# Optimization experiments

Measured on AMD Instinct MI355X. Metric: run time of the kernel, lower is better.

Reference implementation:

```python
import jax, jax.numpy as jnp
import numpy as np

B, S, D, DS = 8, 2048, 1024, 128
TEMP = 1.0
C = 8.0


def setup_inputs() -> dict:
    key = jax.random.key(0)
    ks = jax.random.split(key, 8)
    s_in = 1.0 / np.sqrt(D)
    s_st = 1.0 / np.sqrt(DS)
    return {
        "x": jax.random.normal(ks[0], (B, S, D), jnp.float32),
        "W_k": jax.random.normal(ks[1], (DS, D), jnp.float32) * s_in,
        "W_v": jax.random.normal(ks[2], (DS, D), jnp.float32) * s_in,
        "W_q": jax.random.normal(ks[3], (DS, D), jnp.float32) * s_in,
        "W_alpha_w": jax.random.normal(ks[4], (DS, D), jnp.float32) * s_in,
        "W_alpha_b": jnp.zeros((DS,), jnp.float32),
        "lambda_param": jax.random.uniform(ks[5], (DS,), jnp.float32, 4.0, 9.0),
        "W_o": jax.random.normal(ks[6], (D, DS), jnp.float32) * s_st,
        "norm_weight": jnp.ones((DS,), jnp.float32),
    }


def _l2norm(z):
    # matches F.normalize(..., dim=-1) with eps=1e-12
    n = jnp.linalg.norm(z, axis=-1, keepdims=True)
    return z / jnp.maximum(n, 1e-12)


def reference(x, W_k, W_v, W_q, W_alpha_w, W_alpha_b, lambda_param, W_o, norm_weight):
    # projections
    k = _l2norm(x @ W_k.T)                      # [B,S,DS]
    v = x @ W_v.T                               # [B,S,DS]
    q = _l2norm(x @ W_q.T)                      # [B,S,DS]
    r = jax.nn.sigmoid(x @ W_alpha_w.T + W_alpha_b)
    log_a = jnp.log(jax.nn.sigmoid(lambda_param) + 1e-8)  # [DS]
    alpha = jnp.exp(C * r * log_a)              # [B,S,DS], data-dependent decay

    H0 = jnp.zeros((B, DS, DS), x.dtype)        # state indexed [b, k, v]

    def step(H, inp):
        k_t, v_t, q_t, a_t = inp                # each [B,DS]
        # surprise: prediction error against current state
        pred = jnp.einsum('bk,bkv->bv', q_t, H)
        err = jnp.sum((v_t - pred) ** 2, axis=-1, keepdims=True)  # [B,1]
        sur = jax.nn.sigmoid(err / (TEMP + 1e-6))                 # [B,1]
        # delta rule: k (x) v - k (x) (k^T H) = k (x) (v - k^T H)
        k_proj = jnp.einsum('bk,bkv->bv', k_t, H)
        delta = k_t[:, :, None] * (v_t - k_proj)[:, None, :]      # [B,DS,DS]
        a_e = a_t[:, :, None]                                     # decay on k-axis
        H = a_e * H + (1.0 - a_e) * (sur[:, :, None] * delta)
        y = jnp.einsum('bk,bkv->bv', q_t, H)
        return H, y

    seq = (k.transpose(1, 0, 2), v.transpose(1, 0, 2),
           q.transpose(1, 0, 2), alpha.transpose(1, 0, 2))
    _, ys = jax.lax.scan(step, H0, seq)         # ys: [S,B,DS]
    y = ys.transpose(1, 0, 2)                   # [B,S,DS]

    # RMSNorm (computed in fp32, like the torch module)
    yf = y.astype(jnp.float32)
    yn = yf * jax.lax.rsqrt(jnp.mean(yf * yf, axis=-1, keepdims=True) + 1e-6)
    yn = (yn * norm_weight).astype(y.dtype)
    return yn @ W_o.T                           # [B,S,D]
```

## Files before the change

kernel.cpp:

```cpp
#include <hip/hip_runtime.h>
#include <math.h>

#define S_LEN 2048
#define B_SZ 8
#define D_IN 1024
#define DS_ 128
#define INV_TEMP (1.0f/1.000001f)
#define LBUF 712

#define BAR_LDS() asm volatile("s_waitcnt lgkmcnt(0)\n\ts_barrier" ::: "memory")

#define DPPADD(x, ctrl) { int t_ = __builtin_amdgcn_update_dpp( \
    0, __float_as_int(x), ctrl, 0xF, 0xF, false); x += __int_as_float(t_); }
#define ROWSUM(x) { DPPADD(x, 0x128) DPPADD(x, 0x124) DPPADD(x, 0x122) DPPADD(x, 0x121) }
#define ROWSUM4(v4) { ROWSUM(v4.x) ROWSUM(v4.y) ROWSUM(v4.z) ROWSUM(v4.w) }

__global__ __launch_bounds__(256) void proj_gemm(
    const float* __restrict__ X,
    const float* __restrict__ Wk, const float* __restrict__ Wv,
    const float* __restrict__ Wq, const float* __restrict__ Wa,
    float* __restrict__ P)
{
    __shared__ __align__(16) float As[32][68];
    __shared__ __align__(16) float Bs[32][68];
    const int tid = threadIdx.x;
    const int m0 = blockIdx.x * 64;
    const int n0 = blockIdx.y * 64;
    const int lr = tid >> 3;
    const int lk4 = tid & 7;

    const float* wrows[2];
#pragma unroll
    for (int i = 0; i < 2; i++) {
        int nn = n0 + lr + i * 32;
        const float* w;
        if      (nn < 128) w = Wk + (size_t)nn * D_IN;
        else if (nn < 256) w = Wv + (size_t)(nn - 128) * D_IN;
        else if (nn < 384) w = Wq + (size_t)(nn - 256) * D_IN;
        else               w = Wa + (size_t)(nn - 384) * D_IN;
        wrows[i] = w;
    }
    const int ty = tid >> 4, tx = tid & 15;
    float acc[4][4];
#pragma unroll
    for (int i = 0; i < 4; i++)
#pragma unroll
        for (int j = 0; j < 4; j++) acc[i][j] = 0.f;

    for (int k0 = 0; k0 < D_IN; k0 += 32) {
#pragma unroll
        for (int i = 0; i < 2; i++) {
            int m = lr + i * 32;
            float4 a4 = *(const float4*)(X + (size_t)(m0 + m) * D_IN + k0 + lk4 * 4);
            As[lk4*4+0][m] = a4.x; As[lk4*4+1][m] = a4.y;
            As[lk4*4+2][m] = a4.z; As[lk4*4+3][m] = a4.w;
            float4 b4 = *(const float4*)(wrows[i] + k0 + lk4 * 4);
            Bs[lk4*4+0][m] = b4.x; Bs[lk4*4+1][m] = b4.y;
            Bs[lk4*4+2][m] = b4.z; Bs[lk4*4+3][m] = b4.w;
        }
        __syncthreads();
#pragma unroll
        for (int kk = 0; kk < 32; kk++) {
            float4 a4 = *(const float4*)(&As[kk][ty * 4]);
            float4 b4 = *(const float4*)(&Bs[kk][tx * 4]);
            float a[4] = {a4.x, a4.y, a4.z, a4.w};
            float b[4] = {b4.x, b4.y, b4.z, b4.w};
#pragma unroll
            for (int i = 0; i < 4; i++)
#pragma unroll
                for (int j = 0; j < 4; j++)
                    acc[i][j] = fmaf(a[i], b[j], acc[i][j]);
        }
        __syncthreads();
    }
#pragma unroll
    for (int i = 0; i < 4; i++) {
        float4 o; o.x = acc[i][0]; o.y = acc[i][1]; o.z = acc[i][2]; o.w = acc[i][3];
        *(float4*)(P + (size_t)(m0 + ty * 4 + i) * 512 + n0 + tx * 4) = o;
    }
}

__global__ __launch_bounds__(128) void postproc(
    float* __restrict__ P, float* __restrict__ G,
    const float* __restrict__ bA, const float* __restrict__ lam)
{
    const int tok = blockIdx.x, i = threadIdx.x;
    float* row = P + (size_t)tok * 512;
    float kr = row[i], qr = row[256 + i], rr = row[384 + i];
    float ks = kr * kr, qs = qr * qr;
#pragma unroll
    for (int m = 1; m < 64; m <<= 1) { ks += __shfl_xor(ks, m); qs += __shfl_xor(qs, m); }
    __shared__ float sb[6];
    if ((i & 63) == 0) { sb[(i >> 6) * 2] = ks; sb[(i >> 6) * 2 + 1] = qs; }
    __syncthreads();
    float kinv = 1.0f / fmaxf(sqrtf(sb[0] + sb[2]), 1e-12f);
    float qinv = 1.0f / fmaxf(sqrtf(sb[1] + sb[3]), 1e-12f);
    float kn = kr * kinv, qn = qr * qinv;
    float sr = 1.0f / (1.0f + __expf(-(rr + bA[i])));
    float sl = 1.0f / (1.0f + __expf(-lam[i]));
    float la = logf(sl + 1e-8f);
    float al = __expf(8.0f * sr * la);
    row[i] = kn; row[256 + i] = qn; row[384 + i] = al;
    float gi = qn * (1.0f - al) * kn;
#pragma unroll
    for (int m = 1; m < 64; m <<= 1) gi += __shfl_xor(gi, m);
    if ((i & 63) == 0) sb[4 + (i >> 6)] = gi;
    __syncthreads();
    if (i == 0) G[tok] = sb[4] + sb[5];
}

__global__ __launch_bounds__(512, 2) void recurrence(
    const float* __restrict__ P, const float* __restrict__ G, float* __restrict__ Y)
{
    const int b = blockIdx.x;
    const int tid = threadIdx.x;
    const int c = tid & 15;
    const int vp = tid >> 4;
    const int lane = tid & 63;
    const int wave = tid >> 6;
    const int co = c * 12;

    __shared__ __align__(16) float Pbuf[3][LBUF];
    __shared__ __align__(16) float errw[2][8];

    const float* Pb = P + (size_t)b * S_LEN * 512;
    const float* Gb = G + (size_t)b * S_LEN;
    float* Yb = Y + (size_t)b * S_LEN * DS_;

    float4 H0={0,0,0,0},H1={0,0,0,0},H2={0,0,0,0},H3={0,0,0,0},
           H4={0,0,0,0},H5={0,0,0,0},H6={0,0,0,0},H7={0,0,0,0};

    const bool isP = tid < 256;
    const bool isG = (tid == 256);
    int spos = 0;
    if (isP) {
        int i = tid * 2, s = i >> 7, idx = i & 127, cp = (idx >> 3) * 12 + (idx & 7);
        spos = (s == 0) ? cp : (s == 1) ? (576 + idx) : (s == 2) ? (192 + cp) : (384 + cp);
    }

    float2 rp0 = {0.f, 0.f}, rp1 = {0.f, 0.f};
    float rg0 = 0.f, rg1 = 0.f;
    if (isP) { rp0 = *(const float2*)(Pb + tid * 2); rp1 = *(const float2*)(Pb + 512 + tid * 2); }
    if (isG) { rg0 = Gb[0]; rg1 = Gb[1]; }
    if (isP) *(float2*)(&Pbuf[0][spos]) = rp0;
    if (isG) Pbuf[0][704] = rg0;
    __syncthreads();

#define DOTJ(qs, ks, zs, Hj) { \
    pr.x = fmaf(qs, Hj.x, pr.x); pr.y = fmaf(qs, Hj.y, pr.y); \
    pr.z = fmaf(qs, Hj.z, pr.z); pr.w = fmaf(qs, Hj.w, pr.w); \
    kp.x = fmaf(ks, Hj.x, kp.x); kp.y = fmaf(ks, Hj.y, kp.y); \
    kp.z = fmaf(ks, Hj.z, kp.z); kp.w = fmaf(ks, Hj.w, kp.w); \
    ya.x = fmaf(zs, Hj.x, ya.x); ya.y = fmaf(zs, Hj.y, ya.y); \
    ya.z = fmaf(zs, Hj.z, ya.z); ya.w = fmaf(zs, Hj.w, ya.w); }

#define UPDJ(as_, ws_, Hj) { \
    Hj.x = fmaf(as_, Hj.x, ws_ * sd.x); Hj.y = fmaf(as_, Hj.y, ws_ * sd.y); \
    Hj.z = fmaf(as_, Hj.z, ws_ * sd.z); Hj.w = fmaf(as_, Hj.w, ws_ * sd.w); }

#define STEP(T, PAR, RPS, RGS, RPL, RGL) { \
    float* cb = &Pbuf[(T) % 3][0]; \
    const float4 k0 = *(const float4*)(cb + co); \
    const float4 k1 = *(const float4*)(cb + co + 4); \
    const float4 q0 = *(const float4*)(cb + 192 + co); \
    const float4 q1 = *(const float4*)(cb + 192 + co + 4); \
    const float4 a0 = *(const float4*)(cb + 384 + co); \
    const float4 a1 = *(const float4*)(cb + 384 + co + 4); \
    const float4 vt = *(const float4*)(cb + 576 + vp * 4); \
    const float g = cb[704]; \
    float4 z0, z1, w0, w1; \
    z0.x = q0.x * a0.x; z0.y = q0.y * a0.y; z0.z = q0.z * a0.z; z0.w = q0.w * a0.w; \
    z1.x = q1.x * a1.x; z1.y = q1.y * a1.y; z1.z = q1.z * a1.z; z1.w = q1.w * a1.w; \
    w0.x = fmaf(-k0.x, a0.x, k0.x); w0.y = fmaf(-k0.y, a0.y, k0.y); \
    w0.z = fmaf(-k0.z, a0.z, k0.z); w0.w = fmaf(-k0.w, a0.w, k0.w); \
    w1.x = fmaf(-k1.x, a1.x, k1.x); w1.y = fmaf(-k1.y, a1.y, k1.y); \
    w1.z = fmaf(-k1.z, a1.z, k1.z); w1.w = fmaf(-k1.w, a1.w, k1.w); \
    float4 pr = {0,0,0,0}, kp = {0,0,0,0}, ya = {0,0,0,0}; \
    DOTJ(q0.x, k0.x, z0.x, H0) DOTJ(q0.y, k0.y, z0.y, H1) \
    DOTJ(q0.z, k0.z, z0.z, H2) DOTJ(q0.w, k0.w, z0.w, H3) \
    DOTJ(q1.x, k1.x, z1.x, H4) DOTJ(q1.y, k1.y, z1.y, H5) \
    DOTJ(q1.z, k1.z, z1.z, H6) DOTJ(q1.w, k1.w, z1.w, H7) \
    ROWSUM4(pr) ROWSUM4(kp) ROWSUM4(ya) \
    float4 d4; d4.x = vt.x - kp.x; d4.y = vt.y - kp.y; \
    d4.z = vt.z - kp.z; d4.w = vt.w - kp.w; \
    float ex = vt.x - pr.x, ey = vt.y - pr.y, ez = vt.z - pr.z, ew = vt.w - pr.w; \
    float ep = fmaf(ex, ex, fmaf(ey, ey, fmaf(ez, ez, ew * ew))); \
    ep += __shfl_xor(ep, 16); ep += __shfl_xor(ep, 32); \
    if (lane == 0) errw[PAR][wave] = ep; \
    if ((T) + 1 < S_LEN) { \
        if (isP) *(float2*)(&Pbuf[((T) + 1) % 3][spos]) = RPS; \
        if (isG) Pbuf[((T) + 1) % 3][704] = RGS; } \
    if ((T) + 2 < S_LEN) { \
        if (isP) RPL = *(const float2*)(Pb + (size_t)((T) + 2) * 512 + tid * 2); \
        if (isG) RGL = Gb[(T) + 2]; } \
    BAR_LDS(); \
    const float4 ea = *(const float4*)(&errw[PAR][0]); \
    const float4 eb = *(const float4*)(&errw[PAR][4]); \
    float err = ((ea.x + ea.y) + (ea.z + ea.w)) + ((eb.x + eb.y) + (eb.z + eb.w)); \
    float sur = 1.0f / (1.0f + __expf(-err * INV_TEMP)); \
    float4 sd; sd.x = sur * d4.x; sd.y = sur * d4.y; \
    sd.z = sur * d4.z; sd.w = sur * d4.w; \
    if (c == 0) { \
        float sg = sur * g; float4 y4; \
        y4.x = fmaf(sg, d4.x, ya.x); y4.y = fmaf(sg, d4.y, ya.y); \
        y4.z = fmaf(sg, d4.z, ya.z); y4.w = fmaf(sg, d4.w, ya.w); \
        *(float4*)(Yb + (size_t)(T) * DS_ + vp * 4) = y4; } \
    UPDJ(a0.x, w0.x, H0) UPDJ(a0.y, w0.y, H1) \
    UPDJ(a0.z, w0.z, H2) UPDJ(a0.w, w0.w, H3) \
    UPDJ(a1.x, w1.x, H4) UPDJ(a1.y, w1.y, H5) \
    UPDJ(a1.z, w1.z, H6) UPDJ(a1.w, w1.w, H7) \
}

    for (int t = 0; t < S_LEN; t += 2) {
        STEP(t,     0, rp1, rg1, rp0, rg0)
        STEP(t + 1, 1, rp0, rg0, rp1, rg1)
    }
#undef DOTJ
#undef UPDJ
#undef STEP
}

__global__ __launch_bounds__(128) void rmsnorm(
    float* __restrict__ Y, const float* __restrict__ nw)
{
    const int tok = blockIdx.x, i = threadIdx.x;
    float y = Y[(size_t)tok * DS_ + i];
    float s = y * y;
#pragma unroll
    for (int m = 1; m < 64; m <<= 1) s += __shfl_xor(s, m);
    __shared__ float sb[2];
    if ((i & 63) == 0) sb[i >> 6] = s;
    __syncthreads();
    float ms = (sb[0] + sb[1]) * (1.0f / 128.0f);
    Y[(size_t)tok * DS_ + i] = y * rsqrtf(ms + 1e-6f) * nw[i];
}

__global__ __launch_bounds__(256) void out_gemm(
    const float* __restrict__ Yn, const float* __restrict__ Wo, float* __restrict__ Out)
{
    __shared__ __align__(16) float As[32][68];
    __shared__ __align__(16) float Bs[32][68];
    const int tid = threadIdx.x;
    const int m0 = blockIdx.x * 64;
    const int n0 = blockIdx.y * 64;
    const int lr = tid >> 3;
    const int lk4 = tid & 7;
    const int ty = tid >> 4, tx = tid & 15;
    float acc[4][4];
#pragma unroll
    for (int i = 0; i < 4; i++)
#pragma unroll
        for (int j = 0; j < 4; j++) acc[i][j] = 0.f;

    for (int k0 = 0; k0 < DS_; k0 += 32) {
#pragma unroll
        for (int i = 0; i < 2; i++) {
            int m = lr + i * 32;
            float4 a4 = *(const float4*)(Yn + (size_t)(m0 + m) * DS_ + k0 + lk4 * 4);
            As[lk4*4+0][m] = a4.x; As[lk4*4+1][m] = a4.y;
            As[lk4*4+2][m] = a4.z; As[lk4*4+3][m] = a4.w;
            float4 b4 = *(const float4*)(Wo + (size_t)(n0 + m) * DS_ + k0 + lk4 * 4);
            Bs[lk4*4+0][m] = b4.x; Bs[lk4*4+1][m] = b4.y;
            Bs[lk4*4+2][m] = b4.z; Bs[lk4*4+3][m] = b4.w;
        }
        __syncthreads();
#pragma unroll
        for (int kk = 0; kk < 32; kk++) {
            float4 a4 = *(const float4*)(&As[kk][ty * 4]);
            float4 b4 = *(const float4*)(&Bs[kk][tx * 4]);
            float a[4] = {a4.x, a4.y, a4.z, a4.w};
            float b[4] = {b4.x, b4.y, b4.z, b4.w};
#pragma unroll
            for (int i = 0; i < 4; i++)
#pragma unroll
                for (int j = 0; j < 4; j++)
                    acc[i][j] = fmaf(a[i], b[j], acc[i][j]);
        }
        __syncthreads();
    }
#pragma unroll
    for (int i = 0; i < 4; i++) {
        float4 o; o.x = acc[i][0]; o.y = acc[i][1]; o.z = acc[i][2]; o.w = acc[i][3];
        *(float4*)(Out + (size_t)(m0 + ty * 4 + i) * 1024 + n0 + tx * 4) = o;
    }
}

extern "C" void kernel_launch(void* const* d_in, const int* in_sizes, int n_in,
                              void* d_out, int out_size, void* d_ws, size_t ws_size,
                              hipStream_t stream)
{
    const float* x   = (const float*)d_in[0];
    const float* Wk  = (const float*)d_in[1];
    const float* Wv  = (const float*)d_in[2];
    const float* Wq  = (const float*)d_in[3];
    const float* Waw = (const float*)d_in[4];
    const float* Wab = (const float*)d_in[5];
    const float* lam = (const float*)d_in[6];
    const float* Wo  = (const float*)d_in[7];
    const float* nw  = (const float*)d_in[8];
    float* out = (float*)d_out;

    const size_t NTOK = (size_t)B_SZ * S_LEN;
    float* P  = (float*)d_ws;
    float* G  = P + NTOK * 512;
    float* Y  = G + NTOK;

    proj_gemm<<<dim3(NTOK / 64, 512 / 64), 256, 0, stream>>>(x, Wk, Wv, Wq, Waw, P);
    postproc<<<NTOK, 128, 0, stream>>>(P, G, Wab, lam);
    recurrence<<<B_SZ, 512, 0, stream>>>(P, G, Y);
    rmsnorm<<<NTOK, 128, 0, stream>>>(Y, nw);
    out_gemm<<<dim3(NTOK / 64, 1024 / 64), 256, 0, stream>>>(Y, Wo, out);
}
```

Measured before the change: 2.744 ms.

## Split recurrence across two blocks per batch with cross-block error exchange

```diff
diff --git a/kernel.cpp b/kernel.cpp
--- a/kernel.cpp
+++ b/kernel.cpp
@@ -7,13 +7,13 @@
 #define DS_ 128
 #define INV_TEMP (1.0f/1.000001f)
 #define LBUF 712
+#define NBLK 16
 
 #define BAR_LDS() asm volatile("s_waitcnt lgkmcnt(0)\n\ts_barrier" ::: "memory")
 
 #define DPPADD(x, ctrl) { int t_ = __builtin_amdgcn_update_dpp( \
     0, __float_as_int(x), ctrl, 0xF, 0xF, false); x += __int_as_float(t_); }
 #define ROWSUM(x) { DPPADD(x, 0x128) DPPADD(x, 0x124) DPPADD(x, 0x122) DPPADD(x, 0x121) }
-#define ROWSUM4(v4) { ROWSUM(v4.x) ROWSUM(v4.y) ROWSUM(v4.z) ROWSUM(v4.w) }
 
 __global__ __launch_bounds__(256) void proj_gemm(
     const float* __restrict__ X,
@@ -110,25 +110,32 @@
 }
 
 __global__ __launch_bounds__(512, 2) void recurrence(
-    const float* __restrict__ P, const float* __restrict__ G, float* __restrict__ Y)
-{
-    const int b = blockIdx.x;
+    const float* __restrict__ P, const float* __restrict__ G,
+    float* __restrict__ Y, float* __restrict__ EB)
+{
+    const int bx = blockIdx.x;
+    const int b = bx & 7;
+    const int half = bx >> 3;
     const int tid = threadIdx.x;
     const int c = tid & 15;
     const int vp = tid >> 4;
     const int lane = tid & 63;
     const int wave = tid >> 6;
     const int co = c * 12;
+    const int voff = 576 + half * 64 + vp * 2;
 
     __shared__ __align__(16) float Pbuf[3][LBUF];
     __shared__ __align__(16) float errw[2][8];
 
     const float* Pb = P + (size_t)b * S_LEN * 512;
     const float* Gb = G + (size_t)b * S_LEN;
-    float* Yb = Y + (size_t)b * S_LEN * DS_;
-
-    float4 H0={0,0,0,0},H1={0,0,0,0},H2={0,0,0,0},H3={0,0,0,0},
-           H4={0,0,0,0},H5={0,0,0,0},H6={0,0,0,0},H7={0,0,0,0};
+    float* Yb = Y + (size_t)b * S_LEN * DS_ + half * 64;
+    float* own = EB + (size_t)bx * S_LEN;
+    const float* peer = EB + (size_t)(bx ^ 8) * S_LEN;
+
+    float2 H[8];
+#pragma unroll
+    for (int j = 0; j < 8; j++) { H[j].x = 0.f; H[j].y = 0.f; }
 
     const bool isP = tid < 256;
     const bool isG = (tid == 256);
@@ -146,47 +153,34 @@
     if (isG) Pbuf[0][704] = rg0;
     __syncthreads();
 
-#define DOTJ(qs, ks, zs, Hj) { \
-    pr.x = fmaf(qs, Hj.x, pr.x); pr.y = fmaf(qs, Hj.y, pr.y); \
-    pr.z = fmaf(qs, Hj.z, pr.z); pr.w = fmaf(qs, Hj.w, pr.w); \
-    kp.x = fmaf(ks, Hj.x, kp.x); kp.y = fmaf(ks, Hj.y, kp.y); \
-    kp.z = fmaf(ks, Hj.z, kp.z); kp.w = fmaf(ks, Hj.w, kp.w); \
-    ya.x = fmaf(zs, Hj.x, ya.x); ya.y = fmaf(zs, Hj.y, ya.y); \
-    ya.z = fmaf(zs, Hj.z, ya.z); ya.w = fmaf(zs, Hj.w, ya.w); }
-
-#define UPDJ(as_, ws_, Hj) { \
-    Hj.x = fmaf(as_, Hj.x, ws_ * sd.x); Hj.y = fmaf(as_, Hj.y, ws_ * sd.y); \
-    Hj.z = fmaf(as_, Hj.z, ws_ * sd.z); Hj.w = fmaf(as_, Hj.w, ws_ * sd.w); }
+    float4 k0, k1, q0, q1, a0, a1; float2 vt; float g;
+#define LOADREGS(T) { float* cb = &Pbuf[(T) % 3][0]; \
+    k0 = *(const float4*)(cb + co);       k1 = *(const float4*)(cb + co + 4); \
+    q0 = *(const float4*)(cb + 192 + co); q1 = *(const float4*)(cb + 192 + co + 4); \
+    a0 = *(const float4*)(cb + 384 + co); a1 = *(const float4*)(cb + 384 + co + 4); \
+    vt = *(const float2*)(cb + voff);     g  = cb[704]; }
+
+    LOADREGS(0)
 
 #define STEP(T, PAR, RPS, RGS, RPL, RGL) { \
-    float* cb = &Pbuf[(T) % 3][0]; \
-    const float4 k0 = *(const float4*)(cb + co); \
-    const float4 k1 = *(const float4*)(cb + co + 4); \
-    const float4 q0 = *(const float4*)(cb + 192 + co); \
-    const float4 q1 = *(const float4*)(cb + 192 + co + 4); \
-    const float4 a0 = *(const float4*)(cb + 384 + co); \
-    const float4 a1 = *(const float4*)(cb + 384 + co + 4); \
-    const float4 vt = *(const float4*)(cb + 576 + vp * 4); \
-    const float g = cb[704]; \
-    float4 z0, z1, w0, w1; \
-    z0.x = q0.x * a0.x; z0.y = q0.y * a0.y; z0.z = q0.z * a0.z; z0.w = q0.w * a0.w; \
-    z1.x = q1.x * a1.x; z1.y = q1.y * a1.y; z1.z = q1.z * a1.z; z1.w = q1.w * a1.w; \
-    w0.x = fmaf(-k0.x, a0.x, k0.x); w0.y = fmaf(-k0.y, a0.y, k0.y); \
-    w0.z = fmaf(-k0.z, a0.z, k0.z); w0.w = fmaf(-k0.w, a0.w, k0.w); \
-    w1.x = fmaf(-k1.x, a1.x, k1.x); w1.y = fmaf(-k1.y, a1.y, k1.y); \
-    w1.z = fmaf(-k1.z, a1.z, k1.z); w1.w = fmaf(-k1.w, a1.w, k1.w); \
-    float4 pr = {0,0,0,0}, kp = {0,0,0,0}, ya = {0,0,0,0}; \
-    DOTJ(q0.x, k0.x, z0.x, H0) DOTJ(q0.y, k0.y, z0.y, H1) \
-    DOTJ(q0.z, k0.z, z0.z, H2) DOTJ(q0.w, k0.w, z0.w, H3) \
-    DOTJ(q1.x, k1.x, z1.x, H4) DOTJ(q1.y, k1.y, z1.y, H5) \
-    DOTJ(q1.z, k1.z, z1.z, H6) DOTJ(q1.w, k1.w, z1.w, H7) \
-    ROWSUM4(pr) ROWSUM4(kp) ROWSUM4(ya) \
-    float4 d4; d4.x = vt.x - kp.x; d4.y = vt.y - kp.y; \
-    d4.z = vt.z - kp.z; d4.w = vt.w - kp.w; \
-    float ex = vt.x - pr.x, ey = vt.y - pr.y, ez = vt.z - pr.z, ew = vt.w - pr.w; \
-    float ep = fmaf(ex, ex, fmaf(ey, ey, fmaf(ez, ez, ew * ew))); \
+    float kk[8] = {k0.x,k0.y,k0.z,k0.w,k1.x,k1.y,k1.z,k1.w}; \
+    float qq[8] = {q0.x,q0.y,q0.z,q0.w,q1.x,q1.y,q1.z,q1.w}; \
+    float aa[8] = {a0.x,a0.y,a0.z,a0.w,a1.x,a1.y,a1.z,a1.w}; \
+    float zz[8], ww[8]; \
+    _Pragma("unroll") for (int j = 0; j < 8; j++) { \
+        zz[j] = qq[j] * aa[j]; ww[j] = fmaf(-kk[j], aa[j], kk[j]); } \
+    float2 pr = {0.f,0.f}, kp = {0.f,0.f}, ya = {0.f,0.f}; \
+    _Pragma("unroll") for (int j = 0; j < 8; j++) { \
+        pr.x = fmaf(qq[j], H[j].x, pr.x); pr.y = fmaf(qq[j], H[j].y, pr.y); \
+        kp.x = fmaf(kk[j], H[j].x, kp.x); kp.y = fmaf(kk[j], H[j].y, kp.y); \
+        ya.x = fmaf(zz[j], H[j].x, ya.x); ya.y = fmaf(zz[j], H[j].y, ya.y); } \
+    ROWSUM(pr.x) ROWSUM(pr.y) ROWSUM(kp.x) ROWSUM(kp.y) ROWSUM(ya.x) ROWSUM(ya.y) \
+    float ex = vt.x - pr.x, ey = vt.y - pr.y; \
+    float ep = fmaf(ex, ex, ey * ey); \
     ep += __shfl_xor(ep, 16); ep += __shfl_xor(ep, 32); \
     if (lane == 0) errw[PAR][wave] = ep; \
+    float2 d2; d2.x = vt.x - kp.x; d2.y = vt.y - kp.y; \
+    const float gcur = g; const float2 yac = ya; \
     if ((T) + 1 < S_LEN) { \
         if (isP) *(float2*)(&Pbuf[((T) + 1) % 3][spos]) = RPS; \
         if (isG) Pbuf[((T) + 1) % 3][704] = RGS; } \
@@ -194,30 +188,33 @@
         if (isP) RPL = *(const float2*)(Pb + (size_t)((T) + 2) * 512 + tid * 2); \
         if (isG) RGL = Gb[(T) + 2]; } \
     BAR_LDS(); \
-    const float4 ea = *(const float4*)(&errw[PAR][0]); \
-    const float4 eb = *(const float4*)(&errw[PAR][4]); \
-    float err = ((ea.x + ea.y) + (ea.z + ea.w)) + ((eb.x + eb.y) + (eb.z + eb.w)); \
+    const float4 ea  = *(const float4*)(&errw[PAR][0]); \
+    const float4 eb2 = *(const float4*)(&errw[PAR][4]); \
+    float el = ((ea.x + ea.y) + (ea.z + ea.w)) + ((eb2.x + eb2.y) + (eb2.z + eb2.w)); \
+    if (tid == 0) __hip_atomic_store(own + (T), el + 1.0f, \
+        __ATOMIC_RELAXED, __HIP_MEMORY_SCOPE_AGENT); \
+    _Pragma("unroll") for (int j = 0; j < 8; j++) { H[j].x *= aa[j]; H[j].y *= aa[j]; } \
+    if ((T) + 1 < S_LEN) LOADREGS((T) + 1) \
+    float pv; \
+    do { pv = __hip_atomic_load(peer + (T), \
+        __ATOMIC_RELAXED, __HIP_MEMORY_SCOPE_AGENT); } while (pv == 0.0f); \
+    float err = el + (pv - 1.0f); \
     float sur = 1.0f / (1.0f + __expf(-err * INV_TEMP)); \
-    float4 sd; sd.x = sur * d4.x; sd.y = sur * d4.y; \
-    sd.z = sur * d4.z; sd.w = sur * d4.w; \
+    float2 sd; sd.x = sur * d2.x; sd.y = sur * d2.y; \
+    _Pragma("unroll") for (int j = 0; j < 8; j++) { \
+        H[j].x = fmaf(ww[j], sd.x, H[j].x); H[j].y = fmaf(ww[j], sd.y, H[j].y); } \
     if (c == 0) { \
-        float sg = sur * g; float4 y4; \
-        y4.x = fmaf(sg, d4.x, ya.x); y4.y = fmaf(sg, d4.y, ya.y); \
-        y4.z = fmaf(sg, d4.z, ya.z); y4.w = fmaf(sg, d4.w, ya.w); \
-        *(float4*)(Yb + (size_t)(T) * DS_ + vp * 4) = y4; } \
-    UPDJ(a0.x, w0.x, H0) UPDJ(a0.y, w0.y, H1) \
-    UPDJ(a0.z, w0.z, H2) UPDJ(a0.w, w0.w, H3) \
-    UPDJ(a1.x, w1.x, H4) UPDJ(a1.y, w1.y, H5) \
-    UPDJ(a1.z, w1.z, H6) UPDJ(a1.w, w1.w, H7) \
+        float sg = sur * gcur; float2 y2; \
+        y2.x = fmaf(sg, d2.x, yac.x); y2.y = fmaf(sg, d2.y, yac.y); \
+        *(float2*)(Yb + (size_t)(T) * DS_ + vp * 2) = y2; } \
 }
 
     for (int t = 0; t < S_LEN; t += 2) {
         STEP(t,     0, rp1, rg1, rp0, rg0)
         STEP(t + 1, 1, rp0, rg0, rp1, rg1)
     }
-#undef DOTJ
-#undef UPDJ
 #undef STEP
+#undef LOADREGS
 }
 
 __global__ __launch_bounds__(128) void rmsnorm(
@@ -304,10 +301,12 @@
     float* P  = (float*)d_ws;
     float* G  = P + NTOK * 512;
     float* Y  = G + NTOK;
-
+    float* EB = Y + NTOK * 128;
+
+    hipMemsetAsync(EB, 0, (size_t)NBLK * S_LEN * sizeof(float), stream);
     proj_gemm<<<dim3(NTOK / 64, 512 / 64), 256, 0, stream>>>(x, Wk, Wv, Wq, Waw, P);
     postproc<<<NTOK, 128, 0, stream>>>(P, G, Wab, lam);
-    recurrence<<<B_SZ, 512, 0, stream>>>(P, G, Y);
+    recurrence<<<NBLK, 512, 0, stream>>>(P, G, Y, EB);
     rmsnorm<<<NTOK, 128, 0, stream>>>(Y, nw);
     out_gemm<<<dim3(NTOK / 64, 1024 / 64), 256, 0, stream>>>(Y, Wo, out);
 }
```

Result: slower. 2.985 ms (+8.8%).

## Enlarge GEMM tiles to 128x128 with 8x8 micro-tiles; use permlane swaps in recurrence

Applied to the files above, without the earlier changes.

```diff
diff --git a/kernel.cpp b/kernel.cpp
--- a/kernel.cpp
+++ b/kernel.cpp
@@ -15,68 +15,70 @@
 #define ROWSUM(x) { DPPADD(x, 0x128) DPPADD(x, 0x124) DPPADD(x, 0x122) DPPADD(x, 0x121) }
 #define ROWSUM4(v4) { ROWSUM(v4.x) ROWSUM(v4.y) ROWSUM(v4.z) ROWSUM(v4.w) }
 
+typedef unsigned int uint2v __attribute__((ext_vector_type(2)));
+#define XSUM16(XV) { uint2v r_ = __builtin_amdgcn_permlane16_swap( \
+    __float_as_uint(XV), __float_as_uint(XV), false, false); \
+    XV = __uint_as_float(r_[0]) + __uint_as_float(r_[1]); }
+#define XSUM32(XV) { uint2v r_ = __builtin_amdgcn_permlane32_swap( \
+    __float_as_uint(XV), __float_as_uint(XV), false, false); \
+    XV = __uint_as_float(r_[0]) + __uint_as_float(r_[1]); }
+
 __global__ __launch_bounds__(256) void proj_gemm(
     const float* __restrict__ X,
     const float* __restrict__ Wk, const float* __restrict__ Wv,
     const float* __restrict__ Wq, const float* __restrict__ Wa,
     float* __restrict__ P)
 {
-    __shared__ __align__(16) float As[32][68];
-    __shared__ __align__(16) float Bs[32][68];
+    __shared__ __align__(16) float As[32][132];
+    __shared__ __align__(16) float Bs[32][132];
     const int tid = threadIdx.x;
-    const int m0 = blockIdx.x * 64;
-    const int n0 = blockIdx.y * 64;
-    const int lr = tid >> 3;
-    const int lk4 = tid & 7;
-
-    const float* wrows[2];
-#pragma unroll
-    for (int i = 0; i < 2; i++) {
-        int nn = n0 + lr + i * 32;
-        const float* w;
-        if      (nn < 128) w = Wk + (size_t)nn * D_IN;
-        else if (nn < 256) w = Wv + (size_t)(nn - 128) * D_IN;
-        else if (nn < 384) w = Wq + (size_t)(nn - 256) * D_IN;
-        else               w = Wa + (size_t)(nn - 384) * D_IN;
-        wrows[i] = w;
-    }
+    const int m0 = blockIdx.x * 128;
+    const int n0 = blockIdx.y * 128;
+    const int sr = tid >> 3;
+    const int sk = tid & 7;
+    const float* Wbase = (n0 == 0) ? Wk : (n0 == 128) ? Wv : (n0 == 256) ? Wq : Wa;
     const int ty = tid >> 4, tx = tid & 15;
-    float acc[4][4];
-#pragma unroll
-    for (int i = 0; i < 4; i++)
-#pragma unroll
-        for (int j = 0; j < 4; j++) acc[i][j] = 0.f;
+
+    float acc[8][8];
+#pragma unroll
+    for (int i = 0; i < 8; i++)
+#pragma unroll
+        for (int j = 0; j < 8; j++) acc[i][j] = 0.f;
 
     for (int k0 = 0; k0 < D_IN; k0 += 32) {
 #pragma unroll
-        for (int i = 0; i < 2; i++) {
-            int m = lr + i * 32;
-            float4 a4 = *(const float4*)(X + (size_t)(m0 + m) * D_IN + k0 + lk4 * 4);
-            As[lk4*4+0][m] = a4.x; As[lk4*4+1][m] = a4.y;
-            As[lk4*4+2][m] = a4.z; As[lk4*4+3][m] = a4.w;
-            float4 b4 = *(const float4*)(wrows[i] + k0 + lk4 * 4);
-            Bs[lk4*4+0][m] = b4.x; Bs[lk4*4+1][m] = b4.y;
-            Bs[lk4*4+2][m] = b4.z; Bs[lk4*4+3][m] = b4.w;
+        for (int i = 0; i < 4; i++) {
+            int m = sr + i * 32;
+            float4 a4 = *(const float4*)(X + (size_t)(m0 + m) * D_IN + k0 + sk * 4);
+            As[sk*4+0][m] = a4.x; As[sk*4+1][m] = a4.y;
+            As[sk*4+2][m] = a4.z; As[sk*4+3][m] = a4.w;
+            float4 b4 = *(const float4*)(Wbase + (size_t)m * D_IN + k0 + sk * 4);
+            Bs[sk*4+0][m] = b4.x; Bs[sk*4+1][m] = b4.y;
+            Bs[sk*4+2][m] = b4.z; Bs[sk*4+3][m] = b4.w;
         }
         __syncthreads();
 #pragma unroll
         for (int kk = 0; kk < 32; kk++) {
-            float4 a4 = *(const float4*)(&As[kk][ty * 4]);
-            float4 b4 = *(const float4*)(&Bs[kk][tx * 4]);
-            float a[4] = {a4.x, a4.y, a4.z, a4.w};
-            float b[4] = {b4.x, b4.y, b4.z, b4.w};
-#pragma unroll
-            for (int i = 0; i < 4; i++)
-#pragma unroll
-                for (int j = 0; j < 4; j++)
+            float4 a0 = *(const float4*)(&As[kk][ty * 8]);
+            float4 a1 = *(const float4*)(&As[kk][ty * 8 + 4]);
+            float4 b0 = *(const float4*)(&Bs[kk][tx * 8]);
+            float4 b1 = *(const float4*)(&Bs[kk][tx * 8 + 4]);
+            float a[8] = {a0.x,a0.y,a0.z,a0.w,a1.x,a1.y,a1.z,a1.w};
+            float b[8] = {b0.x,b0.y,b0.z,b0.w,b1.x,b1.y,b1.z,b1.w};
+#pragma unroll
+            for (int i = 0; i < 8; i++)
+#pragma unroll
+                for (int j = 0; j < 8; j++)
                     acc[i][j] = fmaf(a[i], b[j], acc[i][j]);
         }
         __syncthreads();
     }
 #pragma unroll
-    for (int i = 0; i < 4; i++) {
-        float4 o; o.x = acc[i][0]; o.y = acc[i][1]; o.z = acc[i][2]; o.w = acc[i][3];
-        *(float4*)(P + (size_t)(m0 + ty * 4 + i) * 512 + n0 + tx * 4) = o;
+    for (int i = 0; i < 8; i++) {
+        float4 o0; o0.x = acc[i][0]; o0.y = acc[i][1]; o0.z = acc[i][2]; o0.w = acc[i][3];
+        float4 o1; o1.x = acc[i][4]; o1.y = acc[i][5]; o1.z = acc[i][6]; o1.w = acc[i][7];
+        float* dst = P + (size_t)(m0 + ty * 8 + i) * 512 + n0 + tx * 8;
+        *(float4*)(dst) = o0; *(float4*)(dst + 4) = o1;
     }
 }
 
@@ -116,7 +118,6 @@
     const int tid = threadIdx.x;
     const int c = tid & 15;
     const int vp = tid >> 4;
-    const int lane = tid & 63;
     const int wave = tid >> 6;
     const int co = c * 12;
 
@@ -185,8 +186,8 @@
     d4.z = vt.z - kp.z; d4.w = vt.w - kp.w; \
     float ex = vt.x - pr.x, ey = vt.y - pr.y, ez = vt.z - pr.z, ew = vt.w - pr.w; \
     float ep = fmaf(ex, ex, fmaf(ey, ey, fmaf(ez, ez, ew * ew))); \
-    ep += __shfl_xor(ep, 16); ep += __shfl_xor(ep, 32); \
-    if (lane == 0) errw[PAR][wave] = ep; \
+    XSUM16(ep) XSUM32(ep) \
+    if ((tid & 63) == 0) errw[PAR][wave] = ep; \
     if ((T) + 1 < S_LEN) { \
         if (isP) *(float2*)(&Pbuf[((T) + 1) % 3][spos]) = RPS; \
         if (isG) Pbuf[((T) + 1) % 3][704] = RGS; } \
@@ -238,50 +239,55 @@
 __global__ __launch_bounds__(256) void out_gemm(
     const float* __restrict__ Yn, const float* __restrict__ Wo, float* __restrict__ Out)
 {
-    __shared__ __align__(16) float As[32][68];
-    __shared__ __align__(16) float Bs[32][68];
+    __shared__ __align__(16) float As[32][132];
+    __shared__ __align__(16) float Bs[32][132];
     const int tid = threadIdx.x;
-    const int m0 = blockIdx.x * 64;
-    const int n0 = blockIdx.y * 64;
-    const int lr = tid >> 3;
-    const int lk4 = tid & 7;
+    const int m0 = blockIdx.x * 128;
+    const int n0 = blockIdx.y * 128;
+    const int sr = tid >> 3;
+    const int sk = tid & 7;
     const int ty = tid >> 4, tx = tid & 15;
-    float acc[4][4];
-#pragma unroll
-    for (int i = 0; i < 4; i++)
-#pragma unroll
-        for (int j = 0; j < 4; j++) acc[i][j] = 0.f;
+
+    float acc[8][8];
+#pragma unroll
+    for (int i = 0; i < 8; i++)
+#pragma unroll
+        for (int j = 0; j < 8; j++) acc[i][j] = 0.f;
 
     for (int k0 = 0; k0 < DS_; k0 += 32) {
 #pragma unroll
-        for (int i = 0; i < 2; i++) {
-            int m = lr + i * 32;
-            float4 a4 = *(const float4*)(Yn + (size_t)(m0 + m) * DS_ + k0 + lk4 * 4);
-            As[lk4*4+0][m] = a4.x; As[lk4*4+1][m] = a4.y;
-            As[lk4*4+2][m] = a4.z; As[lk4*4+3][m] = a4.w;
-            float4 b4 = *(const float4*)(Wo + (size_t)(n0 + m) * DS_ + k0 + lk4 * 4);
-            Bs[lk4*4+0][m] = b4.x; Bs[lk4*4+1][m] = b4.y;
-            Bs[lk4*4+2][m] = b4.z; Bs[lk4*4+3][m] = b4.w;
+        for (int i = 0; i < 4; i++) {
+            int m = sr + i * 32;
+            float4 a4 = *(const float4*)(Yn + (size_t)(m0 + m) * DS_ + k0 + sk * 4);
+            As[sk*4+0][m] = a4.x; As[sk*4+1][m] = a4.y;
+            As[sk*4+2][m] = a4.z; As[sk*4+3][m] = a4.w;
+            float4 b4 = *(const float4*)(Wo + (size_t)(n0 + m) * DS_ + k0 + sk * 4);
+            Bs[sk*4+0][m] = b4.x; Bs[sk*4+1][m] = b4.y;
+            Bs[sk*4+2][m] = b4.z; Bs[sk*4+3][m] = b4.w;
         }
         __syncthreads();
 #pragma unroll
         for (int kk = 0; kk < 32; kk++) {
-            float4 a4 = *(const float4*)(&As[kk][ty * 4]);
-            float4 b4 = *(const float4*)(&Bs[kk][tx * 4]);
-            float a[4] = {a4.x, a4.y, a4.z, a4.w};
-            float b[4] = {b4.x, b4.y, b4.z, b4.w};
-#pragma unroll
-            for (int i = 0; i < 4; i++)
-#pragma unroll
-                for (int j = 0; j < 4; j++)
+            float4 a0 = *(const float4*)(&As[kk][ty * 8]);
+            float4 a1 = *(const float4*)(&As[kk][ty * 8 + 4]);
+            float4 b0 = *(const float4*)(&Bs[kk][tx * 8]);
+            float4 b1 = *(const float4*)(&Bs[kk][tx * 8 + 4]);
+            float a[8] = {a0.x,a0.y,a0.z,a0.w,a1.x,a1.y,a1.z,a1.w};
+            float b[8] = {b0.x,b0.y,b0.z,b0.w,b1.x,b1.y,b1.z,b1.w};
+#pragma unroll
+            for (int i = 0; i < 8; i++)
+#pragma unroll
+                for (int j = 0; j < 8; j++)
                     acc[i][j] = fmaf(a[i], b[j], acc[i][j]);
         }
         __syncthreads();
     }
 #pragma unroll
-    for (int i = 0; i < 4; i++) {
-        float4 o; o.x = acc[i][0]; o.y = acc[i][1]; o.z = acc[i][2]; o.w = acc[i][3];
-        *(float4*)(Out + (size_t)(m0 + ty * 4 + i) * 1024 + n0 + tx * 4) = o;
+    for (int i = 0; i < 8; i++) {
+        float4 o0; o0.x = acc[i][0]; o0.y = acc[i][1]; o0.z = acc[i][2]; o0.w = acc[i][3];
+        float4 o1; o1.x = acc[i][4]; o1.y = acc[i][5]; o1.z = acc[i][6]; o1.w = acc[i][7];
+        float* dst = Out + (size_t)(m0 + ty * 8 + i) * 1024 + n0 + tx * 8;
+        *(float4*)(dst) = o0; *(float4*)(dst + 4) = o1;
     }
 }
 
@@ -305,9 +311,9 @@
     float* G  = P + NTOK * 512;
     float* Y  = G + NTOK;
 
-    proj_gemm<<<dim3(NTOK / 64, 512 / 64), 256, 0, stream>>>(x, Wk, Wv, Wq, Waw, P);
+    proj_gemm<<<dim3(NTOK / 128, 512 / 128), 256, 0, stream>>>(x, Wk, Wv, Wq, Waw, P);
     postproc<<<NTOK, 128, 0, stream>>>(P, G, Wab, lam);
     recurrence<<<B_SZ, 512, 0, stream>>>(P, G, Y);
     rmsnorm<<<NTOK, 128, 0, stream>>>(Y, nw);
-    out_gemm<<<dim3(NTOK / 64, 1024 / 64), 256, 0, stream>>>(Y, Wo, out);
-}
+    out_gemm<<<dim3(NTOK / 128, 1024 / 128), 256, 0, stream>>>(Y, Wo, out);
+}
```

After: 2.737 ms. No clear change (-0.3%).
